# Performance work log

Measured on AMD Instinct MI355X. Metric: run time of the kernel, lower is better.

## Reference

```python
import jax, jax.numpy as jnp
import numpy as np

N_GAS_NETS = 76  # 29 h2o + 13 o3 + 9 co2 + 3 n2o + 9 ch4 + 13 uniform
N_CHANNELS = 29
N_IN = 2   # (temperature, pressure)
H = 64     # hidden width per n_hidden=[64,64]

# gas index (into composition[0..5]) for each of the 76 stacked nets
COMP_IDX = jnp.asarray(np.repeat(np.arange(6), [29, 13, 9, 3, 9, 13]))

# sparse per-channel combine (hard-coded in the original forward)
H2O_IDX = jnp.asarray([0,1,2,3,4,5,6,3,4,9,10,11,12,13,14,15,16,17,18,19,20,21,22,23,24,25,26,27,28])
O3_CH  = jnp.asarray([0,1,2,17,18,19,20,21,22,25,26,27,28])
CO2_CH = jnp.asarray([0,1,2,5,6,9,10,13,14])
N2O_CH = jnp.asarray([0,1,2])
CH4_CH = jnp.asarray([0,1,2,3,4,7,8,11,12])
U_CH   = jnp.asarray([0,1,2,15,16,17,18,19,20,21,22,27,28])


def setup_inputs() -> dict:
    key = jax.random.key(0)
    ks = jax.random.split(key, 10)
    N = 32768
    t_p = jax.random.normal(ks[0], (N, N_IN), dtype=jnp.float32)
    composition = jax.random.uniform(ks[1], (8, N, 1), dtype=jnp.float32)
    s1 = 1.0 / np.sqrt(N_IN)
    s2 = 1.0 / np.sqrt(H)
    W1 = jax.random.normal(ks[2], (N_GAS_NETS, N_IN, H), dtype=jnp.float32) * s1
    b1 = jnp.zeros((N_GAS_NETS, H), dtype=jnp.float32)
    W2 = jax.random.normal(ks[3], (N_GAS_NETS, H, H), dtype=jnp.float32) * s2
    b2 = jnp.zeros((N_GAS_NETS, H), dtype=jnp.float32)
    Wout = jax.random.normal(ks[4], (N_GAS_NETS, H, 1), dtype=jnp.float32) * s2
    bout = jnp.zeros((N_GAS_NETS, 1), dtype=jnp.float32)
    ke_lw = jax.random.uniform(ks[5], (N_CHANNELS, 1), dtype=jnp.float32)
    ke_iw = jax.random.uniform(ks[6], (N_CHANNELS, 1), dtype=jnp.float32)
    return {"t_p": t_p, "composition": composition, "W1": W1, "b1": b1,
            "W2": W2, "b2": b2, "Wout": Wout, "bout": bout,
            "ke_lw": ke_lw, "ke_iw": ke_iw}


def reference(t_p, composition, W1, b1, W2, b2, Wout, bout, ke_lw, ke_iw):
    # Batched evaluation of all 76 tiny DenseFFN experts on the shared t_p input.
    h = jax.nn.relu(jnp.einsum('ni,gih->gnh', t_p, W1) + b1[:, None, :])   # [76,N,H]
    h = jax.nn.relu(jnp.einsum('gnh,ghk->gnk', h, W2) + b2[:, None, :])    # [76,N,H]
    ke = jax.nn.relu(jnp.einsum('gnh,gho->gno', h, Wout) + bout[:, None, :])  # [76,N,1]

    # tau_gas[gas] = ke * composition[gas_index]
    tau_all = ke * composition[COMP_IDX]  # [76,N,1]
    h2o = tau_all[0:29]
    o3 = tau_all[29:42]
    co2 = tau_all[42:51]
    n2o = tau_all[51:54]
    ch4 = tau_all[54:63]
    u = tau_all[63:76]

    # hard-coded sparse per-channel sum
    tau_gases = h2o[H2O_IDX]                      # [29,N,1]
    tau_gases = tau_gases.at[O3_CH].add(o3)
    tau_gases = tau_gases.at[CO2_CH].add(co2)
    tau_gases = tau_gases.at[N2O_CH].add(n2o)
    tau_gases = tau_gases.at[CH4_CH].add(ch4)
    tau_gases = tau_gases.at[U_CH].add(u)

    tau_lw = ke_lw[:, None, :] * composition[6]   # [29,N,1]
    tau_iw = ke_iw[:, None, :] * composition[7]   # [29,N,1]
    return (tau_gases, tau_lw, tau_iw)
```

## Files before the change

### kernel.cpp

```cpp
#include <hip/hip_runtime.h>

#define NPTS 32768

typedef _Float16 f16;
typedef _Float16 f16x2 __attribute__((ext_vector_type(2)));
typedef _Float16 f16x8 __attribute__((ext_vector_type(8)));
typedef float f32x2 __attribute__((ext_vector_type(2)));
typedef float f32x4 __attribute__((ext_vector_type(4)));
typedef unsigned int u32x4 __attribute__((ext_vector_type(4)));

union U16 { u32x4 u; f32x4 f; f16x2 h2[4]; f16x8 h8; };

static __device__ __forceinline__ f16x2 pk_fma(f16x2 a, f16x2 b, f16x2 c) {
  return __builtin_elementwise_fma(a, b, c);
}
static __device__ __forceinline__ f16x2 pk_relu(f16x2 a) {
  f16x2 z = {(f16)0.f, (f16)0.f};
  return __builtin_elementwise_max(a, z);
}
static __device__ __forceinline__ f16x2 pk_cvt(float a, float b) {
  return __builtin_bit_cast(f16x2, __builtin_amdgcn_cvt_pkrtz(a, b));
}

__device__ const unsigned char G_T[74] = {
  0,0,0,0,0,0,0, 0,0,0,0,0,0,0,0,0,0,0,0,0,0,0,0,0,0,0,0,
  1,1,1,1,1,1,1,1,1,1,1,1,1,
  2,2,2,2,2,2,2,2,2,
  3,3,3,
  4,4,4,4,4,4,4,4,4,
  5,5,5,5,5,5,5,5,5,5,5,5,5
};

__device__ const unsigned char CH_SRC[29][6] = {
  { 0,27,40,49,52,61}, { 1,28,41,50,53,62}, { 2,29,42,51,54,63},
  { 3,55,255,255,255,255}, { 4,56,255,255,255,255},
  { 5,43,255,255,255,255}, { 6,44,255,255,255,255},
  { 3,57,255,255,255,255}, { 4,58,255,255,255,255},
  { 7,45,255,255,255,255}, { 8,46,255,255,255,255},
  { 9,59,255,255,255,255}, {10,60,255,255,255,255},
  {11,47,255,255,255,255}, {12,48,255,255,255,255},
  {13,64,255,255,255,255}, {14,65,255,255,255,255},
  {15,30,66,255,255,255}, {16,31,67,255,255,255}, {17,32,68,255,255,255},
  {18,33,69,255,255,255}, {19,34,70,255,255,255}, {20,35,71,255,255,255},
  {21,255,255,255,255,255}, {22,255,255,255,255,255},
  {23,36,255,255,255,255}, {24,37,255,255,255,255},
  {25,38,72,255,255,255}, {26,39,73,255,255,255}
};
__device__ const unsigned char CH_CNT[29] = {
  6,6,6, 2,2,2,2,2,2,2,2,2,2,2,2,2,2, 3,3,3,3,3,3, 1,1, 2,2, 3,3
};

#define NSLOT 22
#define PACK_SLOTS (74 * NSLOT * 64)

__global__ __launch_bounds__(64) void k0w_pack(
    const float* __restrict__ W1, const float* __restrict__ b1,
    const float* __restrict__ W2, const float* __restrict__ b2,
    const float* __restrict__ Wout, u32x4* __restrict__ pack)
{
  const int gi   = blockIdx.x;
  const int lane = threadIdx.x;
  const int l15  = lane & 15;
  const int quad = lane >> 4;
  const int g    = gi + (gi >= 7 ? 2 : 0);

  const float* W2g = W2 + g * 4096;
  const float* W1g = W1 + g * 128;
  const float* b1g = b1 + g * 64;
  u32x4* dst = pack + gi * NSLOT * 64 + lane;

  #pragma unroll
  for (int mt = 0; mt < 4; ++mt)
    #pragma unroll
    for (int ks = 0; ks < 2; ++ks) {
      U16 u;
      #pragma unroll
      for (int j = 0; j < 4; ++j) {
        const float* s = W2g + (ks * 32 + quad * 8 + 2 * j) * 64 + mt * 16 + l15;
        u.h2[j] = pk_cvt(s[0], s[64]);
      }
      dst[(mt * 2 + ks) * 64] = u.u;
    }
  #pragma unroll
  for (int ks = 0; ks < 2; ++ks) {
    U16 a, b, c;
    #pragma unroll
    for (int j = 0; j < 4; ++j) {
      int h = ks * 32 + quad * 8 + 2 * j;
      a.h2[j] = pk_cvt(W1g[h],      W1g[h + 1]);
      b.h2[j] = pk_cvt(W1g[64 + h], W1g[64 + h + 1]);
      c.h2[j] = pk_cvt(b1g[h],      b1g[h + 1]);
    }
    dst[(8 + ks) * 64]  = a.u;
    dst[(10 + ks) * 64] = b.u;
    dst[(12 + ks) * 64] = c.u;
  }
  #pragma unroll
  for (int mt = 0; mt < 4; ++mt) {
    U16 u, v;
    u.f = *(const f32x4*)(b2   + g * 64 + mt * 16 + quad * 4);
    v.f = *(const f32x4*)(Wout + g * 64 + mt * 16 + quad * 4);
    dst[(14 + mt) * 64] = u.u;
    dst[(18 + mt) * 64] = v.u;
  }
}

__global__ __launch_bounds__(256, 2) void k1_mlp(
    const float* __restrict__ t_p, const float* __restrict__ comp,
    const u32x4* __restrict__ pack, const float* __restrict__ bout,
    float* __restrict__ planes)
{
  const int lane = threadIdx.x & 63;
  const int l15  = lane & 15;
  const int quad = lane >> 4;
  const int w    = blockIdx.x * 4 + (threadIdx.x >> 6);
  const int gi   = w >> 6;
  const int g    = gi + (gi >= 7 ? 2 : 0);
  const int pb0  = (w & 63) * 512;

  const int t  = G_T[gi];

  const bool qb0 = (quad & 1) != 0;
  const bool qb1 = (quad & 2) != 0;

  const u32x4* pksrc = pack + gi * NSLOT * 64 + lane;
  f16x8 afrag[4][2];
  f32x4 b2q[4];
  f32x2 wq2[4][2];
  #pragma unroll
  for (int mt = 0; mt < 4; ++mt) {
    afrag[mt][0] = __builtin_bit_cast(f16x8, pksrc[(mt * 2 + 0) * 64]);
    afrag[mt][1] = __builtin_bit_cast(f16x8, pksrc[(mt * 2 + 1) * 64]);
    b2q[mt] = __builtin_bit_cast(f32x4, pksrc[(14 + mt) * 64]);
    f32x4 wv = __builtin_bit_cast(f32x4, pksrc[(18 + mt) * 64]);
    wq2[mt][0] = f32x2{ wv[0], wv[1] };
    wq2[mt][1] = f32x2{ wv[2], wv[3] };
  }
  U16 w0s[2], w1s[2], b1s[2];
  #pragma unroll
  for (int ks = 0; ks < 2; ++ks) {
    w0s[ks].u = pksrc[(8 + ks) * 64];
    w1s[ks].u = pksrc[(10 + ks) * 64];
    b1s[ks].u = pksrc[(12 + ks) * 64];
  }
  const float bo = bout[g];

  const float2* tp2 = (const float2*)t_p;
  const float* compt = comp + t * NPTS;
  float* plane = planes + gi * NPTS;

  float2 xv_n[4];
  float cv_n;
  #pragma unroll
  for (int pt = 0; pt < 4; ++pt)
    xv_n[pt] = tp2[pb0 + pt * 16 + l15];
  cv_n = compt[pb0 + lane];

  #pragma unroll
  for (int pass = 0; pass < 8; ++pass) {
    const int pb = pb0 + pass * 64;

    float2 xv[4];
    #pragma unroll
    for (int pt = 0; pt < 4; ++pt) xv[pt] = xv_n[pt];
    const float cv = cv_n;

    if (pass < 7) {
      const int pbn = pb + 64;
      #pragma unroll
      for (int pt = 0; pt < 4; ++pt)
        xv_n[pt] = tp2[pbn + pt * 16 + l15];
      cv_n = compt[pbn + lane];
    }

    f16x2 x0v[4], x1v[4];
    #pragma unroll
    for (int pt = 0; pt < 4; ++pt) {
      x0v[pt] = pk_cvt(xv[pt].x, xv[pt].x);
      x1v[pt] = pk_cvt(xv[pt].y, xv[pt].y);
    }

    U16 bfrag[2][4];
    #pragma unroll
    for (int ks = 0; ks < 2; ++ks)
      #pragma unroll
      for (int pt = 0; pt < 4; ++pt)
        #pragma unroll
        for (int i = 0; i < 4; ++i)
          bfrag[ks][pt].h2[i] =
              pk_relu(pk_fma(x0v[pt], w0s[ks].h2[i],
                             pk_fma(x1v[pt], w1s[ks].h2[i], b1s[ks].h2[i])));

    f32x2 p2[4];
    #pragma unroll
    for (int pt = 0; pt < 4; ++pt) p2[pt] = f32x2{ 0.f, 0.f };

    #pragma unroll
    for (int mt = 0; mt < 4; ++mt) {
      f32x4 c[4];
      #pragma unroll
      for (int pt = 0; pt < 4; ++pt)
        c[pt] = __builtin_amdgcn_mfma_f32_16x16x32_f16(
            afrag[mt][0], bfrag[0][pt].h8, b2q[mt], 0, 0, 0);
      #pragma unroll
      for (int pt = 0; pt < 4; ++pt)
        c[pt] = __builtin_amdgcn_mfma_f32_16x16x32_f16(
            afrag[mt][1], bfrag[1][pt].h8, c[pt], 0, 0, 0);
      #pragma unroll
      for (int pt = 0; pt < 4; ++pt) {
        f32x2 z = { 0.f, 0.f };
        f32x2 a0 = { c[pt][0], c[pt][1] };
        f32x2 a1 = { c[pt][2], c[pt][3] };
        a0 = __builtin_elementwise_max(a0, z);
        a1 = __builtin_elementwise_max(a1, z);
        p2[pt] = __builtin_elementwise_fma(a0, wq2[mt][0], p2[pt]);
        p2[pt] = __builtin_elementwise_fma(a1, wq2[mt][1], p2[pt]);
      }
    }

    float p[4];
    #pragma unroll
    for (int pt = 0; pt < 4; ++pt) p[pt] = p2[pt][0] + p2[pt][1];

    float u  = qb1 ? (qb0 ? p[3] : p[2]) : (qb0 ? p[1] : p[0]);
    float v  = qb1 ? (qb0 ? p[2] : p[3]) : (qb0 ? p[0] : p[1]);
    float w2 = qb1 ? (qb0 ? p[1] : p[0]) : (qb0 ? p[3] : p[2]);
    float x  = qb1 ? (qb0 ? p[0] : p[1]) : (qb0 ? p[2] : p[3]);
    float s  = u + __shfl_xor(v, 16, 64);
    float tt = w2 + __shfl_xor(x, 16, 64);
    float r  = s + __shfl_xor(tt, 32, 64);

    float tau = fmaxf(r + bo, 0.f) * cv;
    plane[pb + lane] = tau;
  }
}

__global__ __launch_bounds__(256) void k2_gather(
    const float* __restrict__ planes, const float* __restrict__ comp,
    const float* __restrict__ ke_lw, const float* __restrict__ ke_iw,
    float* __restrict__ out)
{
  const int c  = blockIdx.x >> 5;
  const int n  = (((blockIdx.x & 31) << 8) + threadIdx.x) * 4;

  const int cnt = CH_CNT[c];
  f32x4 acc = *(const f32x4*)(planes + (int)CH_SRC[c][0] * NPTS + n);
  for (int j = 1; j < cnt; ++j)
    acc += *(const f32x4*)(planes + (int)CH_SRC[c][j] * NPTS + n);
  *(f32x4*)(out + c * NPTS + n) = acc;

  f32x4 c6 = *(const f32x4*)(comp + 6 * NPTS + n);
  f32x4 c7 = *(const f32x4*)(comp + 7 * NPTS + n);
  *(f32x4*)(out + (29 + c) * NPTS + n) = c6 * ke_lw[c];
  *(f32x4*)(out + (58 + c) * NPTS + n) = c7 * ke_iw[c];
}

extern "C" void kernel_launch(void* const* d_in, const int* in_sizes, int n_in,
                              void* d_out, int out_size, void* d_ws, size_t ws_size,
                              hipStream_t stream)
{
  const float* t_p   = (const float*)d_in[0];
  const float* comp  = (const float*)d_in[1];
  const float* W1    = (const float*)d_in[2];
  const float* b1    = (const float*)d_in[3];
  const float* W2    = (const float*)d_in[4];
  const float* b2    = (const float*)d_in[5];
  const float* Wout  = (const float*)d_in[6];
  const float* bout  = (const float*)d_in[7];
  const float* ke_lw = (const float*)d_in[8];
  const float* ke_iw = (const float*)d_in[9];
  float* out = (float*)d_out;

  u32x4* pack   = (u32x4*)d_ws;
  float* planes = (float*)(pack + PACK_SLOTS);

  k0w_pack<<<74, 64, 0, stream>>>(W1, b1, W2, b2, Wout, pack);
  k1_mlp<<<1184, 256, 0, stream>>>(t_p, comp, pack, bout, planes);
  k2_gather<<<29 * 32, 256, 0, stream>>>(planes, comp, ke_lw, ke_iw, out);
}
```

Measured before the change: 117.1 us.

## Stage MLP weights in LDS and halve points per pass to raise occupancy

```diff
diff --git a/kernel.cpp b/kernel.cpp
--- a/kernel.cpp
+++ b/kernel.cpp
@@ -105,133 +105,121 @@
   }
 }
 
-__global__ __launch_bounds__(256, 2) void k1_mlp(
+__global__ __launch_bounds__(256, 4) void k1_mlp(
     const float* __restrict__ t_p, const float* __restrict__ comp,
     const u32x4* __restrict__ pack, const float* __restrict__ bout,
     float* __restrict__ planes)
 {
-  const int lane = threadIdx.x & 63;
+  __shared__ u32x4 wlds[NSLOT * 64];
+
+  const int tid  = threadIdx.x;
+  const int lane = tid & 63;
   const int l15  = lane & 15;
   const int quad = lane >> 4;
-  const int w    = blockIdx.x * 4 + (threadIdx.x >> 6);
+  const int wid  = tid >> 6;
+  const int w    = blockIdx.x * 4 + wid;
   const int gi   = w >> 6;
   const int g    = gi + (gi >= 7 ? 2 : 0);
   const int pb0  = (w & 63) * 512;
-
-  const int t  = G_T[gi];
-
-  const bool qb0 = (quad & 1) != 0;
-  const bool qb1 = (quad & 2) != 0;
-
-  const u32x4* pksrc = pack + gi * NSLOT * 64 + lane;
-  f16x8 afrag[4][2];
-  f32x4 b2q[4];
+  const int t    = G_T[gi];
+
+  {
+    const u32x4* psrc = pack + gi * (NSLOT * 64);
+    #pragma unroll
+    for (int s = wid; s < NSLOT; s += 4)
+      wlds[s * 64 + lane] = psrc[s * 64 + lane];
+  }
+  __syncthreads();
+
+  U16 w0s[2], w1s[2], b1s[2];
+  #pragma unroll
+  for (int ks = 0; ks < 2; ++ks) {
+    w0s[ks].u = wlds[(8 + ks) * 64 + lane];
+    w1s[ks].u = wlds[(10 + ks) * 64 + lane];
+    b1s[ks].u = wlds[(12 + ks) * 64 + lane];
+  }
   f32x2 wq2[4][2];
   #pragma unroll
   for (int mt = 0; mt < 4; ++mt) {
-    afrag[mt][0] = __builtin_bit_cast(f16x8, pksrc[(mt * 2 + 0) * 64]);
-    afrag[mt][1] = __builtin_bit_cast(f16x8, pksrc[(mt * 2 + 1) * 64]);
-    b2q[mt] = __builtin_bit_cast(f32x4, pksrc[(14 + mt) * 64]);
-    f32x4 wv = __builtin_bit_cast(f32x4, pksrc[(18 + mt) * 64]);
+    f32x4 wv = __builtin_bit_cast(f32x4, wlds[(18 + mt) * 64 + lane]);
     wq2[mt][0] = f32x2{ wv[0], wv[1] };
     wq2[mt][1] = f32x2{ wv[2], wv[3] };
   }
-  U16 w0s[2], w1s[2], b1s[2];
-  #pragma unroll
-  for (int ks = 0; ks < 2; ++ks) {
-    w0s[ks].u = pksrc[(8 + ks) * 64];
-    w1s[ks].u = pksrc[(10 + ks) * 64];
-    b1s[ks].u = pksrc[(12 + ks) * 64];
-  }
   const float bo = bout[g];
 
-  const float2* tp2 = (const float2*)t_p;
+  const float2* tp2  = (const float2*)t_p;
   const float* compt = comp + t * NPTS;
   float* plane = planes + gi * NPTS;
 
-  float2 xv_n[4];
-  float cv_n;
-  #pragma unroll
-  for (int pt = 0; pt < 4; ++pt)
-    xv_n[pt] = tp2[pb0 + pt * 16 + l15];
-  cv_n = compt[pb0 + lane];
-
-  #pragma unroll
-  for (int pass = 0; pass < 8; ++pass) {
-    const int pb = pb0 + pass * 64;
-
-    float2 xv[4];
-    #pragma unroll
-    for (int pt = 0; pt < 4; ++pt) xv[pt] = xv_n[pt];
-    const float cv = cv_n;
-
-    if (pass < 7) {
-      const int pbn = pb + 64;
-      #pragma unroll
-      for (int pt = 0; pt < 4; ++pt)
-        xv_n[pt] = tp2[pbn + pt * 16 + l15];
-      cv_n = compt[pbn + lane];
-    }
-
-    f16x2 x0v[4], x1v[4];
-    #pragma unroll
-    for (int pt = 0; pt < 4; ++pt) {
-      x0v[pt] = pk_cvt(xv[pt].x, xv[pt].x);
-      x1v[pt] = pk_cvt(xv[pt].y, xv[pt].y);
-    }
-
-    U16 bfrag[2][4];
+  const bool qb0 = (quad & 1) != 0;
+  const int  l31 = lane & 31;
+
+  float2 xv_n0 = tp2[pb0 + l15];
+  float2 xv_n1 = tp2[pb0 + 16 + l15];
+  float  cv_n  = compt[pb0 + l31];
+
+  #pragma unroll 2
+  for (int pass = 0; pass < 16; ++pass) {
+    const int pb = pb0 + pass * 32;
+
+    const float2 xv0 = xv_n0;
+    const float2 xv1 = xv_n1;
+    const float  cv  = cv_n;
+
+    if (pass < 15) {
+      xv_n0 = tp2[pb + 32 + l15];
+      xv_n1 = tp2[pb + 48 + l15];
+      cv_n  = compt[pb + 32 + l31];
+    }
+
+    const f16x2 x0v[2] = { pk_cvt(xv0.x, xv0.x), pk_cvt(xv1.x, xv1.x) };
+    const f16x2 x1v[2] = { pk_cvt(xv0.y, xv0.y), pk_cvt(xv1.y, xv1.y) };
+
+    U16 bfrag[2][2];
     #pragma unroll
     for (int ks = 0; ks < 2; ++ks)
       #pragma unroll
-      for (int pt = 0; pt < 4; ++pt)
+      for (int pt = 0; pt < 2; ++pt)
         #pragma unroll
         for (int i = 0; i < 4; ++i)
           bfrag[ks][pt].h2[i] =
               pk_relu(pk_fma(x0v[pt], w0s[ks].h2[i],
                              pk_fma(x1v[pt], w1s[ks].h2[i], b1s[ks].h2[i])));
 
-    f32x2 p2[4];
-    #pragma unroll
-    for (int pt = 0; pt < 4; ++pt) p2[pt] = f32x2{ 0.f, 0.f };
+    f32x2 p2[2] = { f32x2{0.f, 0.f}, f32x2{0.f, 0.f} };
 
     #pragma unroll
     for (int mt = 0; mt < 4; ++mt) {
-      f32x4 c[4];
-      #pragma unroll
-      for (int pt = 0; pt < 4; ++pt)
-        c[pt] = __builtin_amdgcn_mfma_f32_16x16x32_f16(
-            afrag[mt][0], bfrag[0][pt].h8, b2q[mt], 0, 0, 0);
-      #pragma unroll
-      for (int pt = 0; pt < 4; ++pt)
-        c[pt] = __builtin_amdgcn_mfma_f32_16x16x32_f16(
-            afrag[mt][1], bfrag[1][pt].h8, c[pt], 0, 0, 0);
-      #pragma unroll
-      for (int pt = 0; pt < 4; ++pt) {
-        f32x2 z = { 0.f, 0.f };
-        f32x2 a0 = { c[pt][0], c[pt][1] };
-        f32x2 a1 = { c[pt][2], c[pt][3] };
-        a0 = __builtin_elementwise_max(a0, z);
-        a1 = __builtin_elementwise_max(a1, z);
-        p2[pt] = __builtin_elementwise_fma(a0, wq2[mt][0], p2[pt]);
-        p2[pt] = __builtin_elementwise_fma(a1, wq2[mt][1], p2[pt]);
-      }
-    }
-
-    float p[4];
-    #pragma unroll
-    for (int pt = 0; pt < 4; ++pt) p[pt] = p2[pt][0] + p2[pt][1];
-
-    float u  = qb1 ? (qb0 ? p[3] : p[2]) : (qb0 ? p[1] : p[0]);
-    float v  = qb1 ? (qb0 ? p[2] : p[3]) : (qb0 ? p[0] : p[1]);
-    float w2 = qb1 ? (qb0 ? p[1] : p[0]) : (qb0 ? p[3] : p[2]);
-    float x  = qb1 ? (qb0 ? p[0] : p[1]) : (qb0 ? p[2] : p[3]);
-    float s  = u + __shfl_xor(v, 16, 64);
-    float tt = w2 + __shfl_xor(x, 16, 64);
-    float r  = s + __shfl_xor(tt, 32, 64);
-
-    float tau = fmaxf(r + bo, 0.f) * cv;
-    plane[pb + lane] = tau;
+      const f16x8 af0 = __builtin_bit_cast(f16x8, wlds[(mt * 2 + 0) * 64 + lane]);
+      const f16x8 af1 = __builtin_bit_cast(f16x8, wlds[(mt * 2 + 1) * 64 + lane]);
+      const f32x4 bq  = __builtin_bit_cast(f32x4, wlds[(14 + mt) * 64 + lane]);
+
+      f32x4 c0 = __builtin_amdgcn_mfma_f32_16x16x32_f16(af0, bfrag[0][0].h8, bq, 0, 0, 0);
+      f32x4 c1 = __builtin_amdgcn_mfma_f32_16x16x32_f16(af0, bfrag[0][1].h8, bq, 0, 0, 0);
+      c0 = __builtin_amdgcn_mfma_f32_16x16x32_f16(af1, bfrag[1][0].h8, c0, 0, 0, 0);
+      c1 = __builtin_amdgcn_mfma_f32_16x16x32_f16(af1, bfrag[1][1].h8, c1, 0, 0, 0);
+
+      const f32x2 z = { 0.f, 0.f };
+      f32x2 a00 = __builtin_elementwise_max(f32x2{ c0[0], c0[1] }, z);
+      f32x2 a01 = __builtin_elementwise_max(f32x2{ c0[2], c0[3] }, z);
+      f32x2 a10 = __builtin_elementwise_max(f32x2{ c1[0], c1[1] }, z);
+      f32x2 a11 = __builtin_elementwise_max(f32x2{ c1[2], c1[3] }, z);
+      p2[0] = __builtin_elementwise_fma(a00, wq2[mt][0], p2[0]);
+      p2[0] = __builtin_elementwise_fma(a01, wq2[mt][1], p2[0]);
+      p2[1] = __builtin_elementwise_fma(a10, wq2[mt][0], p2[1]);
+      p2[1] = __builtin_elementwise_fma(a11, wq2[mt][1], p2[1]);
+    }
+
+    const float pA = p2[0][0] + p2[0][1];
+    const float pB = p2[1][0] + p2[1][1];
+
+    const float sA = qb0 ? pB : pA;
+    const float sB = qb0 ? pA : pB;
+    const float x1 = sA + __shfl_xor(sB, 16, 64);
+    const float r  = x1 + __shfl_xor(x1, 32, 64);
+
+    const float tau = fmaxf(r + bo, 0.f) * cv;
+    if (quad < 2) plane[pb + l31] = tau;
   }
 }
 
```

After: 127.3 us. 8.8% more time.

## Stage W2 fragments in LDS, halve per-wave work, raise occupancy

Applied to the files above, without the earlier changes.

```diff
diff --git a/kernel.cpp b/kernel.cpp
--- a/kernel.cpp
+++ b/kernel.cpp
@@ -105,37 +105,33 @@
   }
 }
 
-__global__ __launch_bounds__(256, 2) void k1_mlp(
+__global__ __launch_bounds__(256, 3) void k1_mlp(
     const float* __restrict__ t_p, const float* __restrict__ comp,
     const u32x4* __restrict__ pack, const float* __restrict__ bout,
     float* __restrict__ planes)
 {
-  const int lane = threadIdx.x & 63;
+  __shared__ u32x4 wlds[12 * 64];
+
+  const int tid  = threadIdx.x;
+  const int lane = tid & 63;
   const int l15  = lane & 15;
   const int quad = lane >> 4;
-  const int w    = blockIdx.x * 4 + (threadIdx.x >> 6);
-  const int gi   = w >> 6;
+  const int wid  = tid >> 6;
+  const int w    = blockIdx.x * 4 + wid;
+  const int gi   = w >> 7;
   const int g    = gi + (gi >= 7 ? 2 : 0);
-  const int pb0  = (w & 63) * 512;
-
-  const int t  = G_T[gi];
-
-  const bool qb0 = (quad & 1) != 0;
-  const bool qb1 = (quad & 2) != 0;
-
-  const u32x4* pksrc = pack + gi * NSLOT * 64 + lane;
-  f16x8 afrag[4][2];
-  f32x4 b2q[4];
-  f32x2 wq2[4][2];
-  #pragma unroll
-  for (int mt = 0; mt < 4; ++mt) {
-    afrag[mt][0] = __builtin_bit_cast(f16x8, pksrc[(mt * 2 + 0) * 64]);
-    afrag[mt][1] = __builtin_bit_cast(f16x8, pksrc[(mt * 2 + 1) * 64]);
-    b2q[mt] = __builtin_bit_cast(f32x4, pksrc[(14 + mt) * 64]);
-    f32x4 wv = __builtin_bit_cast(f32x4, pksrc[(18 + mt) * 64]);
-    wq2[mt][0] = f32x2{ wv[0], wv[1] };
-    wq2[mt][1] = f32x2{ wv[2], wv[3] };
-  }
+  const int pb0  = (w & 127) * 256;
+  const int t    = G_T[gi];
+
+  const u32x4* psrc = pack + gi * (NSLOT * 64);
+
+  #pragma unroll
+  for (int s = wid; s < 12; s += 4) {
+    const int gs = s < 8 ? s : s + 6;
+    wlds[s * 64 + lane] = psrc[gs * 64 + lane];
+  }
+
+  const u32x4* pksrc = psrc + lane;
   U16 w0s[2], w1s[2], b1s[2];
   #pragma unroll
   for (int ks = 0; ks < 2; ++ks) {
@@ -143,11 +139,23 @@
     w1s[ks].u = pksrc[(10 + ks) * 64];
     b1s[ks].u = pksrc[(12 + ks) * 64];
   }
+  f32x2 wq2[4][2];
+  #pragma unroll
+  for (int mt = 0; mt < 4; ++mt) {
+    f32x4 wv = __builtin_bit_cast(f32x4, pksrc[(18 + mt) * 64]);
+    wq2[mt][0] = f32x2{ wv[0], wv[1] };
+    wq2[mt][1] = f32x2{ wv[2], wv[3] };
+  }
   const float bo = bout[g];
 
-  const float2* tp2 = (const float2*)t_p;
+  __syncthreads();
+
+  const float2* tp2  = (const float2*)t_p;
   const float* compt = comp + t * NPTS;
   float* plane = planes + gi * NPTS;
+
+  const bool qb0 = (quad & 1) != 0;
+  const bool qb1 = (quad & 2) != 0;
 
   float2 xv_n[4];
   float cv_n;
@@ -157,7 +165,7 @@
   cv_n = compt[pb0 + lane];
 
   #pragma unroll
-  for (int pass = 0; pass < 8; ++pass) {
+  for (int pass = 0; pass < 4; ++pass) {
     const int pb = pb0 + pass * 64;
 
     float2 xv[4];
@@ -165,7 +173,7 @@
     for (int pt = 0; pt < 4; ++pt) xv[pt] = xv_n[pt];
     const float cv = cv_n;
 
-    if (pass < 7) {
+    if (pass < 3) {
       const int pbn = pb + 64;
       #pragma unroll
       for (int pt = 0; pt < 4; ++pt)
@@ -197,22 +205,23 @@
 
     #pragma unroll
     for (int mt = 0; mt < 4; ++mt) {
+      const f16x8 af0 = __builtin_bit_cast(f16x8, wlds[(mt * 2 + 0) * 64 + lane]);
+      const f16x8 af1 = __builtin_bit_cast(f16x8, wlds[(mt * 2 + 1) * 64 + lane]);
+      const f32x4 bq  = __builtin_bit_cast(f32x4, wlds[(8 + mt) * 64 + lane]);
+
       f32x4 c[4];
       #pragma unroll
       for (int pt = 0; pt < 4; ++pt)
-        c[pt] = __builtin_amdgcn_mfma_f32_16x16x32_f16(
-            afrag[mt][0], bfrag[0][pt].h8, b2q[mt], 0, 0, 0);
-      #pragma unroll
-      for (int pt = 0; pt < 4; ++pt)
-        c[pt] = __builtin_amdgcn_mfma_f32_16x16x32_f16(
-            afrag[mt][1], bfrag[1][pt].h8, c[pt], 0, 0, 0);
+        c[pt] = __builtin_amdgcn_mfma_f32_16x16x32_f16(af0, bfrag[0][pt].h8, bq, 0, 0, 0);
+      #pragma unroll
+      for (int pt = 0; pt < 4; ++pt)
+        c[pt] = __builtin_amdgcn_mfma_f32_16x16x32_f16(af1, bfrag[1][pt].h8, c[pt], 0, 0, 0);
+
       #pragma unroll
       for (int pt = 0; pt < 4; ++pt) {
-        f32x2 z = { 0.f, 0.f };
-        f32x2 a0 = { c[pt][0], c[pt][1] };
-        f32x2 a1 = { c[pt][2], c[pt][3] };
-        a0 = __builtin_elementwise_max(a0, z);
-        a1 = __builtin_elementwise_max(a1, z);
+        const f32x2 z = { 0.f, 0.f };
+        f32x2 a0 = __builtin_elementwise_max(f32x2{ c[pt][0], c[pt][1] }, z);
+        f32x2 a1 = __builtin_elementwise_max(f32x2{ c[pt][2], c[pt][3] }, z);
         p2[pt] = __builtin_elementwise_fma(a0, wq2[mt][0], p2[pt]);
         p2[pt] = __builtin_elementwise_fma(a1, wq2[mt][1], p2[pt]);
       }
@@ -230,7 +239,7 @@
     float tt = w2 + __shfl_xor(x, 16, 64);
     float r  = s + __shfl_xor(tt, 32, 64);
 
-    float tau = fmaxf(r + bo, 0.f) * cv;
+    const float tau = fmaxf(r + bo, 0.f) * cv;
     plane[pb + lane] = tau;
   }
 }
@@ -275,6 +284,6 @@
   float* planes = (float*)(pack + PACK_SLOTS);
 
   k0w_pack<<<74, 64, 0, stream>>>(W1, b1, W2, b2, Wout, pack);
-  k1_mlp<<<1184, 256, 0, stream>>>(t_p, comp, pack, bout, planes);
+  k1_mlp<<<2368, 256, 0, stream>>>(t_p, comp, pack, bout, planes);
   k2_gather<<<29 * 32, 256, 0, stream>>>(planes, comp, ke_lw, ke_iw, out);
 }
```

New measurement: 116.3 us. Within noise of the previous version (-0.6%).
